# Kernel tuning notes

Measured on AMD Instinct MI355X. Metric: run time of the kernel, lower is better.

Reference implementation:

```python
import jax, jax.numpy as jnp
import numpy as np

B, S, OBS, D, H, F, L, A = 64, 512, 128, 512, 8, 2048, 4, 16
KERNEL_EPS = 1e-3  # performer kernel_epsilon
LN_EPS = 1e-6      # flax LayerNorm default


def _layernorm(x, s, b):
    m = jnp.mean(x, axis=-1, keepdims=True)
    v = jnp.mean(jnp.square(x - m), axis=-1, keepdims=True)
    return (x - m) * jax.lax.rsqrt(v + LN_EPS) * s + b


def _favor_attn(x, Wq, bq, Wk, bk, Wv, bv, Wo, bo):
    # FAVOR+ generalized attention, deterministic relu features, bidirectional,
    # renormalize_attention=True. phi(u) = relu(u) + kernel_epsilon.
    Bx, Sx, Dx = x.shape
    hd = Dx // H
    q = (x @ Wq + bq).reshape(Bx, Sx, H, hd)
    k = (x @ Wk + bk).reshape(Bx, Sx, H, hd)
    v = (x @ Wv + bv).reshape(Bx, Sx, H, hd)
    pq = jax.nn.relu(q) + KERNEL_EPS  # [B,S,H,m]
    pk = jax.nn.relu(k) + KERNEL_EPS
    kv = jnp.einsum('bshm,bshd->bhmd', pk, v)      # [B,H,m,hd]
    num = jnp.einsum('bshm,bhmd->bshd', pq, kv)    # [B,S,H,hd]
    ksum = jnp.sum(pk, axis=1)                      # [B,H,m]
    den = jnp.einsum('bshm,bhm->bsh', pq, ksum)    # [B,S,H]
    out = num / den[..., None]
    return out.reshape(Bx, Sx, Dx) @ Wo + bo


def setup_inputs() -> dict:
    key = jax.random.key(0)
    ks = jax.random.split(key, 32)
    sc = lambda *shape: 0.02
    inp = {
        'hidden_state': jax.random.normal(ks[0], (B, 1, D), jnp.float32),
        'ins': jax.random.normal(ks[1], (B, S, OBS), jnp.float32),
        'resets': jax.random.randint(ks[2], (B,), 0, 2) > 0,
        'W_emb': jax.random.normal(ks[3], (OBS, D), jnp.float32) * 0.02,
        'b_emb': jnp.zeros((D,), jnp.float32),
        'Wq': jax.random.normal(ks[4], (L, D, D), jnp.float32) * 0.02,
        'bq': jnp.zeros((L, D), jnp.float32),
        'Wk': jax.random.normal(ks[5], (L, D, D), jnp.float32) * 0.02,
        'bk': jnp.zeros((L, D), jnp.float32),
        'Wv': jax.random.normal(ks[6], (L, D, D), jnp.float32) * 0.02,
        'bv': jnp.zeros((L, D), jnp.float32),
        'Wo': jax.random.normal(ks[7], (L, D, D), jnp.float32) * 0.02,
        'bo': jnp.zeros((L, D), jnp.float32),
        'ln1_s': jnp.ones((L, D), jnp.float32),
        'ln1_b': jnp.zeros((L, D), jnp.float32),
        'ln2_s': jnp.ones((L, D), jnp.float32),
        'ln2_b': jnp.zeros((L, D), jnp.float32),
        'W1': jax.random.normal(ks[8], (L, D, F), jnp.float32) * 0.02,
        'b1': jnp.zeros((L, F), jnp.float32),
        'W2': jax.random.normal(ks[9], (L, F, D), jnp.float32) * 0.02,
        'b2': jnp.zeros((L, D), jnp.float32),
        'W_qp': jax.random.normal(ks[10], (D, A), jnp.float32) * 0.02,
        'b_qp': jnp.zeros((A,), jnp.float32),
    }
    return inp


def reference(hidden_state, ins, resets, W_emb, b_emb, Wq, bq, Wk, bk, Wv, bv,
              Wo, bo, ln1_s, ln1_b, ln2_s, ln2_b, W1, b1, W2, b2, W_qp, b_qp):
    emb = ins @ W_emb + b_emb                                   # [B,S,D]
    h0 = jnp.where(resets[:, None, None], jnp.zeros_like(hidden_state), hidden_state)
    x = jnp.concatenate([h0, emb], axis=1)                      # [B,S+1,D]
    for l in range(Wq.shape[0]):
        att = _favor_attn(x, Wq[l], bq[l], Wk[l], bk[l], Wv[l], bv[l], Wo[l], bo[l])
        x = _layernorm(att + x, ln1_s[l], ln1_b[l])
        ff = jax.nn.relu(x @ W1[l] + b1[l]) @ W2[l] + b2[l]
        x = _layernorm(ff + x, ln2_s[l], ln2_b[l])
    h_out = x[:, 0:1, :]                                        # [B,1,D]
    q_vals = h_out @ W_qp + b_qp                                # [B,1,A]
    return (h_out, q_vals)
```

## Files before the change

### kernel.cpp

```cpp
#include <hip/hip_runtime.h>

typedef __bf16 bf16;
typedef __bf16 bf16x8 __attribute__((ext_vector_type(8)));
typedef float  f32x4  __attribute__((ext_vector_type(4)));


__device__ __forceinline__ void cp16(const bf16* g, bf16* l)
{
    __builtin_amdgcn_global_load_lds(
        (const __attribute__((address_space(1))) void*)g,
        (__attribute__((address_space(3))) void*)l,
        16, 0, 0);
}

__global__ __launch_bounds__(256) void cvt_bf16(
    const float* __restrict__ src, bf16* __restrict__ dst, int n)
{
    for (int i = blockIdx.x * 256 + threadIdx.x; i < n; i += gridDim.x * 256)
        dst[i] = (bf16)src[i];
}

__global__ __launch_bounds__(256) void transpose_f32(
    const float* __restrict__ W, bf16* __restrict__ WT, int K, int N, long elemOff)
{
    __shared__ bf16 tile[32][33];
    const int bn = blockIdx.x * 32;
    const int bk = blockIdx.y * 32;
    const int tx = threadIdx.x & 31, ty = threadIdx.x >> 5;
    for (int r = 0; r < 32; r += 8)
        tile[ty + r][tx] = (bf16)W[elemOff + (long)(bk + ty + r) * N + (bn + tx)];
    __syncthreads();
    for (int r = 0; r < 32; r += 8)
        WT[(long)(bn + ty + r) * K + (bk + tx)] = tile[tx][ty + r];
}

__global__ __launch_bounds__(256) void build_x0(
    const float* __restrict__ hs, const int* __restrict__ resets,
    bf16* __restrict__ xb)
{
    const int b = blockIdx.x;
    const bool rz = (resets[b] != 0);
    const long base = (long)b * 513 * 512;
    for (int d = threadIdx.x; d < 512; d += 256)
        xb[base + d] = rz ? (bf16)0.f : (bf16)hs[b * 512 + d];
}

__global__ __launch_bounds__(256) void concat3(
    const float* __restrict__ a, const float* __restrict__ b,
    const float* __restrict__ c, float* __restrict__ d)
{
    const int i = blockIdx.x * 256 + threadIdx.x;
    if (i < 512)       d[i] = a[i];
    else if (i < 1024) d[i] = b[i - 512];
    else if (i < 1536) d[i] = c[i - 1024];
}

template<int ROWMAP, int ACT>
__global__ __launch_bounds__(256) void gemm128(
    const bf16* __restrict__ A, const bf16* __restrict__ BT,
    const float* __restrict__ bias, bf16* __restrict__ outB,
    int M, int N, int K, int lda, int ldc)
{
    __shared__ bf16 As[128 * 32];
    __shared__ bf16 Bs[128 * 32];
    const int tid  = threadIdx.x;
    const int wave = tid >> 6;
    const int lane = tid & 63;
    const int q    = lane >> 4;
    const int lm   = lane & 15;
    const int wr   = wave >> 1, wc = wave & 1;

    int flat;
    {
        const int nwg  = gridDim.x * gridDim.y;
        const int orig = blockIdx.y * gridDim.x + blockIdx.x;
        const int qq = nwg >> 3, rr = nwg & 7;
        const int xcd = orig & 7, idx = orig >> 3;
        flat = (xcd < rr ? xcd * (qq + 1) : rr * (qq + 1) + (xcd - rr) * qq) + idx;
    }
    const int bx = flat % gridDim.x;
    const int by = flat / gridDim.x;
    int m0 = by * 128;
    if (m0 > M - 128) m0 = M - 128;
    const int n0 = bx * 128;

    const int r0 = wave * 32 + (lane >> 2);
    const int ks = (lane & 3) * 8;
    const bf16* Ag0 = A  + (long)(m0 + r0) * lda + ks;
    const bf16* Ag1 = A  + (long)(m0 + r0 + 16) * lda + ks;
    const bf16* Bg0 = BT + (long)(n0 + r0) * K + ks;
    const bf16* Bg1 = BT + (long)(n0 + r0 + 16) * K + ks;
    bf16* Al0 = As + wave * 1024;
    bf16* Al1 = As + wave * 1024 + 512;
    bf16* Bl0 = Bs + wave * 1024;
    bf16* Bl1 = Bs + wave * 1024 + 512;

    f32x4 acc[4][4];
    for (int i = 0; i < 4; i++) for (int j = 0; j < 4; j++)
        for (int r = 0; r < 4; r++) acc[i][j][r] = 0.f;

    for (int k0 = 0; k0 < K; k0 += 32) {
        cp16(Ag0 + k0, Al0);
        cp16(Ag1 + k0, Al1);
        cp16(Bg0 + k0, Bl0);
        cp16(Bg1 + k0, Bl1);
        __syncthreads();
        bf16x8 af[4], bfr[4];
        #pragma unroll
        for (int i = 0; i < 4; i++)
            af[i] = *(const bf16x8*)(As + (wr * 64 + i * 16 + lm) * 32 + q * 8);
        #pragma unroll
        for (int j = 0; j < 4; j++)
            bfr[j] = *(const bf16x8*)(Bs + (wc * 64 + j * 16 + lm) * 32 + q * 8);
        #pragma unroll
        for (int i = 0; i < 4; i++)
            #pragma unroll
            for (int j = 0; j < 4; j++)
                acc[i][j] = __builtin_amdgcn_mfma_f32_16x16x32_bf16(
                    af[i], bfr[j], acc[i][j], 0, 0, 0);
        __syncthreads();
    }

    #pragma unroll
    for (int j = 0; j < 4; j++) {
        const int col = n0 + wc * 64 + j * 16 + lm;
        const float bv = bias[col];
        #pragma unroll
        for (int i = 0; i < 4; i++) {
            #pragma unroll
            for (int r = 0; r < 4; r++) {
                int row = m0 + wr * 64 + i * 16 + q * 4 + r;
                float vv = acc[i][j][r] + bv;
                if (ACT == 1) vv = fmaxf(vv, 0.f);
                if (ACT == 2) vv = fmaxf(vv, 0.f) + 1e-3f;
                if (ACT == 3 && col < 1024) vv = fmaxf(vv, 0.f) + 1e-3f;
                if (ROWMAP == 1) row = row + (row >> 9) + 1;
                outB[(long)row * ldc + col] = (bf16)vv;
            }
        }
    }
}

#define FP 72
__global__ __launch_bounds__(256) void favor_mfma(bf16* qkv)
{
    const int bh = blockIdx.x;
    const int b = bh >> 3, h = bh & 7;
    const long rbQ = (long)b * 513 * 1536 + h * 64;
    const long rbK = rbQ + 512;
    const long rbV = rbQ + 1024;

    __shared__ bf16 pkT[64][FP];
    __shared__ bf16 vT [64][FP];
    __shared__ bf16 kvT[64][FP];
    __shared__ bf16 pqS[64][FP];
    __shared__ float ksumS[64];
    __shared__ float denS[64];

    const int tid  = threadIdx.x;
    const int wave = tid >> 6;
    const int lane = tid & 63;
    const int q    = lane >> 4;
    const int lm   = lane & 15;
    const int wr   = wave >> 1, wc = wave & 1;
    const int mp   = (tid & 31) * 2;
    const int sr   = tid >> 5;

    if (tid < 64) ksumS[tid] = 0.f;
    float ksp0 = 0.f, ksp1 = 0.f;

    f32x4 akv[2][2];
    for (int i = 0; i < 2; i++) for (int j = 0; j < 2; j++)
        for (int r = 0; r < 4; r++) akv[i][j][r] = 0.f;

    for (int t8 = 0; t8 < 9; t8++) {
        const int s0 = t8 * 64;
        #pragma unroll
        for (int i = 0; i < 8; i++) {
            const int s  = sr + i * 8;
            const int gs = s0 + s;
            unsigned pkw = 0, vw = 0;
            if (gs < 513) {
                pkw = *(const unsigned*)(qkv + rbK + (long)gs * 1536 + mp);
                vw  = *(const unsigned*)(qkv + rbV + (long)gs * 1536 + mp);
            }
            union { unsigned u; bf16 hh[2]; } pu, vu;
            pu.u = pkw; vu.u = vw;
            pkT[mp][s]     = pu.hh[0];
            pkT[mp + 1][s] = pu.hh[1];
            vT[mp][s]      = vu.hh[0];
            vT[mp + 1][s]  = vu.hh[1];
            ksp0 += (float)pu.hh[0];
            ksp1 += (float)pu.hh[1];
        }
        __syncthreads();
        #pragma unroll
        for (int ks = 0; ks < 2; ks++) {
            bf16x8 a0 = *(const bf16x8*)(&pkT[wr * 32 + lm     ][ks * 32 + q * 8]);
            bf16x8 a1 = *(const bf16x8*)(&pkT[wr * 32 + 16 + lm][ks * 32 + q * 8]);
            bf16x8 b0 = *(const bf16x8*)(&vT [wc * 32 + lm     ][ks * 32 + q * 8]);
            bf16x8 b1 = *(const bf16x8*)(&vT [wc * 32 + 16 + lm][ks * 32 + q * 8]);
            akv[0][0] = __builtin_amdgcn_mfma_f32_16x16x32_bf16(a0, b0, akv[0][0], 0, 0, 0);
            akv[0][1] = __builtin_amdgcn_mfma_f32_16x16x32_bf16(a0, b1, akv[0][1], 0, 0, 0);
            akv[1][0] = __builtin_amdgcn_mfma_f32_16x16x32_bf16(a1, b0, akv[1][0], 0, 0, 0);
            akv[1][1] = __builtin_amdgcn_mfma_f32_16x16x32_bf16(a1, b1, akv[1][1], 0, 0, 0);
        }
        __syncthreads();
    }
    atomicAdd(&ksumS[mp],     ksp0);
    atomicAdd(&ksumS[mp + 1], ksp1);
    #pragma unroll
    for (int i = 0; i < 2; i++)
        #pragma unroll
        for (int j = 0; j < 2; j++)
            #pragma unroll
            for (int r = 0; r < 4; r++)
                kvT[wc * 32 + j * 16 + lm][wr * 32 + i * 16 + q * 4 + r] =
                    (bf16)akv[i][j][r];
    __syncthreads();

    const int prow = tid >> 2;
    const int pseg = (tid & 3) * 16;
    for (int t8 = 0; t8 < 9; t8++) {
        const int s0 = t8 * 64;
        const int gs = s0 + prow;
        if (gs < 513) {
            *(bf16x8*)(&pqS[prow][pseg])     = *(const bf16x8*)(qkv + rbQ + (long)gs * 1536 + pseg);
            *(bf16x8*)(&pqS[prow][pseg + 8]) = *(const bf16x8*)(qkv + rbQ + (long)gs * 1536 + pseg + 8);
        } else {
            bf16x8 z;
            for (int r = 0; r < 8; r++) z[r] = (bf16)0.f;
            *(bf16x8*)(&pqS[prow][pseg])     = z;
            *(bf16x8*)(&pqS[prow][pseg + 8]) = z;
        }
        __syncthreads();
        {
            const int s = tid >> 2, mb = (tid & 3) * 16;
            float dp = 0.f;
            #pragma unroll
            for (int m2 = 0; m2 < 16; m2++)
                dp += (float)pqS[s][mb + m2] * ksumS[mb + m2];
            dp += __shfl_xor(dp, 1);
            dp += __shfl_xor(dp, 2);
            if ((tid & 3) == 0) denS[s] = dp;
        }
        __syncthreads();
        f32x4 an[4];
        for (int j = 0; j < 4; j++)
            for (int r = 0; r < 4; r++) an[j][r] = 0.f;
        #pragma unroll
        for (int ks = 0; ks < 2; ks++) {
            bf16x8 a = *(const bf16x8*)(&pqS[wave * 16 + lm][ks * 32 + q * 8]);
            #pragma unroll
            for (int j = 0; j < 4; j++) {
                bf16x8 bb = *(const bf16x8*)(&kvT[j * 16 + lm][ks * 32 + q * 8]);
                an[j] = __builtin_amdgcn_mfma_f32_16x16x32_bf16(a, bb, an[j], 0, 0, 0);
            }
        }
        #pragma unroll
        for (int j = 0; j < 4; j++) {
            #pragma unroll
            for (int r = 0; r < 4; r++) {
                const int sl  = wave * 16 + q * 4 + r;
                const int gs2 = s0 + sl;
                if (gs2 < 513) {
                    const int d = j * 16 + lm;
                    qkv[rbQ + (long)gs2 * 1536 + d] = (bf16)(an[j][r] / denS[sl]);
                }
            }
        }
        __syncthreads();
    }
}

__global__ __launch_bounds__(256) void ln_res(
    const bf16* __restrict__ y, int ldy, const float* __restrict__ sc,
    const float* __restrict__ bi, bf16* __restrict__ xb)
{
    const int row  = blockIdx.x * 4 + (threadIdx.x >> 6);
    const int lane = threadIdx.x & 63;
    const bf16* yr = y  + (long)row * ldy + lane * 8;
    bf16*       xr = xb + (long)row * 512 + lane * 8;
    bf16x8 yv = *(const bf16x8*)yr;
    bf16x8 xv = *(const bf16x8*)xr;
    float v[8];
    float sum = 0.f;
    #pragma unroll
    for (int i = 0; i < 8; i++) { v[i] = (float)yv[i] + (float)xv[i]; sum += v[i]; }
    #pragma unroll
    for (int o = 32; o; o >>= 1) sum += __shfl_xor(sum, o);
    const float mean = sum * (1.f / 512.f);
    float vs = 0.f;
    #pragma unroll
    for (int i = 0; i < 8; i++) { float dd = v[i] - mean; vs += dd * dd; }
    #pragma unroll
    for (int o = 32; o; o >>= 1) vs += __shfl_xor(vs, o);
    const float rstd = rsqrtf(vs * (1.f / 512.f) + 1e-6f);
    bf16x8 ov;
    #pragma unroll
    for (int i = 0; i < 8; i++)
        ov[i] = (bf16)((v[i] - mean) * rstd * sc[lane * 8 + i] + bi[lane * 8 + i]);
    *(bf16x8*)xr = ov;
}

__global__ __launch_bounds__(256) void final_head(
    const bf16* __restrict__ xb, const float* __restrict__ Wqp,
    const float* __restrict__ bqp, float* __restrict__ out)
{
    const int b = blockIdx.x;
    const bf16* xr = xb + (long)b * 513 * 512;
    for (int i = threadIdx.x; i < 512; i += 256) out[b * 512 + i] = (float)xr[i];
    const int a = threadIdx.x & 15, g = threadIdx.x >> 4;
    float p = 0.f;
    for (int k = g * 32; k < g * 32 + 32; k++)
        p += (float)xr[k] * Wqp[k * 16 + a];
    __shared__ float red[256];
    red[threadIdx.x] = p;
    __syncthreads();
    if (threadIdx.x < 16) {
        float s = bqp[a];
        for (int g2 = 0; g2 < 16; g2++) s += red[g2 * 16 + a];
        out[64 * 512 + b * 16 + a] = s;
    }
}

extern "C" void kernel_launch(void* const* d_in, const int* in_sizes, int n_in,
                              void* d_out, int out_size, void* d_ws, size_t ws_size,
                              hipStream_t stream)
{
    (void)in_sizes; (void)n_in; (void)out_size; (void)ws_size;
    const float* hs    = (const float*)d_in[0];
    const float* ins   = (const float*)d_in[1];
    const int*   resets= (const int*)d_in[2];
    const float* W_emb = (const float*)d_in[3];
    const float* b_emb = (const float*)d_in[4];
    const float* Wq    = (const float*)d_in[5];
    const float* bq    = (const float*)d_in[6];
    const float* Wk    = (const float*)d_in[7];
    const float* bk    = (const float*)d_in[8];
    const float* Wv    = (const float*)d_in[9];
    const float* bv    = (const float*)d_in[10];
    const float* Wo    = (const float*)d_in[11];
    const float* bo    = (const float*)d_in[12];
    const float* ln1s  = (const float*)d_in[13];
    const float* ln1b  = (const float*)d_in[14];
    const float* ln2s  = (const float*)d_in[15];
    const float* ln2b  = (const float*)d_in[16];
    const float* W1    = (const float*)d_in[17];
    const float* b1    = (const float*)d_in[18];
    const float* W2    = (const float*)d_in[19];
    const float* b2    = (const float*)d_in[20];
    const float* Wqp   = (const float*)d_in[21];
    const float* bqp   = (const float*)d_in[22];
    float* out = (float*)d_out;
    char* ws  = (char*)d_ws;

    bf16* xb   = (bf16*)(ws);
    bf16* qkv  = (bf16*)(ws + 33619968);
    bf16* f    = qkv;
    bf16* y2   = (bf16*)(ws + 33619968 + 67239936);
    bf16* WembT= (bf16*)(ws + 134479872);
    char* LW   = ws + 134610944;
    bf16* WqkvT= (bf16*)(LW + 0);
    bf16* WoT  = (bf16*)(LW + 1572864);
    bf16* W1T  = (bf16*)(LW + 2097152);
    bf16* W2T  = (bf16*)(LW + 4194304);
    float* bqkv= (float*)(LW + 6291456);
    bf16* insb = (bf16*)(ws + 140908544);

    cvt_bf16<<<4096, 256, 0, stream>>>(ins, insb, 4194304);
    transpose_f32<<<dim3(16, 4), 256, 0, stream>>>(W_emb, WembT, 128, 512, 0);
    build_x0<<<64, 256, 0, stream>>>(hs, resets, xb);
    gemm128<1, 0><<<dim3(4, 256), 256, 0, stream>>>(
        insb, WembT, b_emb, xb, 32768, 512, 128, 128, 512);

    for (int l = 0; l < 4; l++) {
        const long o512  = (long)l * 262144;
        const long o2048 = (long)l * 1048576;
        transpose_f32<<<dim3(16, 16), 256, 0, stream>>>(Wq, WqkvT,          512, 512,  o512);
        transpose_f32<<<dim3(16, 16), 256, 0, stream>>>(Wk, WqkvT + 262144, 512, 512,  o512);
        transpose_f32<<<dim3(16, 16), 256, 0, stream>>>(Wv, WqkvT + 524288, 512, 512,  o512);
        transpose_f32<<<dim3(16, 16), 256, 0, stream>>>(Wo, WoT,            512, 512,  o512);
        transpose_f32<<<dim3(64, 16), 256, 0, stream>>>(W1, W1T,            512, 2048, o2048);
        transpose_f32<<<dim3(16, 64), 256, 0, stream>>>(W2, W2T,            2048, 512, o2048);
        concat3<<<6, 256, 0, stream>>>(bq + l * 512, bk + l * 512, bv + l * 512, bqkv);

        gemm128<0, 3><<<dim3(12, 257), 256, 0, stream>>>(
            xb, WqkvT, bqkv, qkv, 32832, 1536, 512, 512, 1536);
        favor_mfma<<<512, 256, 0, stream>>>(qkv);
        gemm128<0, 0><<<dim3(4, 257), 256, 0, stream>>>(
            qkv, WoT, bo + l * 512, qkv + 512, 32832, 512, 512, 1536, 1536);
        ln_res<<<8208, 256, 0, stream>>>(qkv + 512, 1536, ln1s + l * 512, ln1b + l * 512, xb);

        for (int c = 0; c < 2; c++) {
            const long r0 = (long)c * 16416;
            gemm128<0, 1><<<dim3(16, 129), 256, 0, stream>>>(
                xb + r0 * 512, W1T, b1 + l * 2048, f, 16416, 2048, 512, 512, 2048);
            gemm128<0, 0><<<dim3(4, 129), 256, 0, stream>>>(
                f, W2T, b2 + l * 512, y2 + r0 * 512, 16416, 512, 2048, 2048, 512);
        }
        ln_res<<<8208, 256, 0, stream>>>(y2, 512, ln2s + l * 512, ln2b + l * 512, xb);
    }

    final_head<<<64, 256, 0, stream>>>(xb, Wqp, bqp, out);
}
```

Measured before the change: 1.906 ms.

## Widen GEMM K-tile to 64 and batch per-layer weight prep launches

The bf16 MFMA GEMM now stages 64-wide K tiles per iteration: eight async global-to-LDS copies per wave and two MFMA sub-steps between barriers. This halves the number of loop iterations and barriers and keeps more loads in flight. The per-layer weight transposes are merged into two z-indexed launches, and the QKV bias concat is hoisted into a single launch over all layers, reusing the WembT scratch area once the embedding GEMM is done. The GEMM doubles its LDS use, and the 128-byte LDS row stride may add bank conflicts on fragment reads.

```diff
diff --git a/kernel.cpp b/kernel.cpp
--- a/kernel.cpp
+++ b/kernel.cpp
@@ -32,6 +32,63 @@
     __syncthreads();
     for (int r = 0; r < 32; r += 8)
         WT[(long)(bn + ty + r) * K + (bk + tx)] = tile[tx][ty + r];
+}
+
+__global__ __launch_bounds__(256) void prep_qkvo(
+    const float* __restrict__ Wq, const float* __restrict__ Wk,
+    const float* __restrict__ Wv, const float* __restrict__ Wo,
+    bf16* __restrict__ WqkvT, bf16* __restrict__ WoT, long elemOff)
+{
+    __shared__ bf16 tile[32][33];
+    const int z = blockIdx.z;
+    const float* W = (z == 0) ? Wq : (z == 1) ? Wk : (z == 2) ? Wv : Wo;
+    bf16* WT = (z < 3) ? (WqkvT + (long)z * 262144) : WoT;
+    const int bn = blockIdx.x * 32;
+    const int bk = blockIdx.y * 32;
+    const int tx = threadIdx.x & 31, ty = threadIdx.x >> 5;
+    for (int r = 0; r < 32; r += 8)
+        tile[ty + r][tx] = (bf16)W[elemOff + (long)(bk + ty + r) * 512 + (bn + tx)];
+    __syncthreads();
+    for (int r = 0; r < 32; r += 8)
+        WT[(long)(bn + ty + r) * 512 + (bk + tx)] = tile[tx][ty + r];
+}
+
+__global__ __launch_bounds__(256) void prep_ffn(
+    const float* __restrict__ W1, const float* __restrict__ W2,
+    bf16* __restrict__ W1T, bf16* __restrict__ W2T, long elemOff)
+{
+    __shared__ bf16 tile[32][33];
+    const int z = blockIdx.z;
+    const float* W = z ? W2 : W1;
+    bf16* WT = z ? W2T : W1T;
+    const int N = z ? 512 : 2048;
+    const int K = z ? 2048 : 512;
+    const int bn = (z ? blockIdx.y : blockIdx.x) * 32;
+    const int bk = (z ? blockIdx.x : blockIdx.y) * 32;
+    const int tx = threadIdx.x & 31, ty = threadIdx.x >> 5;
+    for (int r = 0; r < 32; r += 8)
+        tile[ty + r][tx] = (bf16)W[elemOff + (long)(bk + ty + r) * N + (bn + tx)];
+    __syncthreads();
+    for (int r = 0; r < 32; r += 8)
+        WT[(long)(bn + ty + r) * K + (bk + tx)] = tile[tx][ty + r];
+}
+
+__global__ __launch_bounds__(256) void concat_all(
+    const float* __restrict__ bq, const float* __restrict__ bk,
+    const float* __restrict__ bv, float* __restrict__ dst)
+{
+    const int i = blockIdx.x * 256 + threadIdx.x;
+    const int l = i >> 11;
+    int rem = i;
+    int lay = 0;
+    while (rem >= 1536) { rem -= 1536; lay++; }
+    if (lay > 3) return;
+    float v;
+    if (rem < 512)        v = bq[lay * 512 + rem];
+    else if (rem < 1024)  v = bk[lay * 512 + rem - 512];
+    else                  v = bv[lay * 512 + rem - 1024];
+    dst[lay * 1536 + rem] = v;
+    (void)l;
 }
 
 __global__ __launch_bounds__(256) void build_x0(
@@ -45,24 +102,14 @@
         xb[base + d] = rz ? (bf16)0.f : (bf16)hs[b * 512 + d];
 }
 
-__global__ __launch_bounds__(256) void concat3(
-    const float* __restrict__ a, const float* __restrict__ b,
-    const float* __restrict__ c, float* __restrict__ d)
-{
-    const int i = blockIdx.x * 256 + threadIdx.x;
-    if (i < 512)       d[i] = a[i];
-    else if (i < 1024) d[i] = b[i - 512];
-    else if (i < 1536) d[i] = c[i - 1024];
-}
-
 template<int ROWMAP, int ACT>
 __global__ __launch_bounds__(256) void gemm128(
     const bf16* __restrict__ A, const bf16* __restrict__ BT,
     const float* __restrict__ bias, bf16* __restrict__ outB,
     int M, int N, int K, int lda, int ldc)
 {
-    __shared__ bf16 As[128 * 32];
-    __shared__ bf16 Bs[128 * 32];
+    __shared__ bf16 As[128 * 64];
+    __shared__ bf16 Bs[128 * 64];
     const int tid  = threadIdx.x;
     const int wave = tid >> 6;
     const int lane = tid & 63;
@@ -84,40 +131,42 @@
     if (m0 > M - 128) m0 = M - 128;
     const int n0 = bx * 128;
 
-    const int r0 = wave * 32 + (lane >> 2);
-    const int ks = (lane & 3) * 8;
-    const bf16* Ag0 = A  + (long)(m0 + r0) * lda + ks;
-    const bf16* Ag1 = A  + (long)(m0 + r0 + 16) * lda + ks;
-    const bf16* Bg0 = BT + (long)(n0 + r0) * K + ks;
-    const bf16* Bg1 = BT + (long)(n0 + r0 + 16) * K + ks;
-    bf16* Al0 = As + wave * 1024;
-    bf16* Al1 = As + wave * 1024 + 512;
-    bf16* Bl0 = Bs + wave * 1024;
-    bf16* Bl1 = Bs + wave * 1024 + 512;
+    const int srow = lane >> 3;
+    const int scol = (lane & 7) * 8;
+    const bf16* Ag = A  + (long)(m0 + wave * 32 + srow) * lda + scol;
+    const bf16* Bg = BT + (long)(n0 + wave * 32 + srow) * K   + scol;
+    const long lda8 = (long)lda * 8;
+    const long K8   = (long)K * 8;
+    bf16* Al = As + wave * 2048;
+    bf16* Bl = Bs + wave * 2048;
 
     f32x4 acc[4][4];
     for (int i = 0; i < 4; i++) for (int j = 0; j < 4; j++)
         for (int r = 0; r < 4; r++) acc[i][j][r] = 0.f;
 
-    for (int k0 = 0; k0 < K; k0 += 32) {
-        cp16(Ag0 + k0, Al0);
-        cp16(Ag1 + k0, Al1);
-        cp16(Bg0 + k0, Bl0);
-        cp16(Bg1 + k0, Bl1);
-        __syncthreads();
-        bf16x8 af[4], bfr[4];
-        #pragma unroll
-        for (int i = 0; i < 4; i++)
-            af[i] = *(const bf16x8*)(As + (wr * 64 + i * 16 + lm) * 32 + q * 8);
-        #pragma unroll
-        for (int j = 0; j < 4; j++)
-            bfr[j] = *(const bf16x8*)(Bs + (wc * 64 + j * 16 + lm) * 32 + q * 8);
-        #pragma unroll
-        for (int i = 0; i < 4; i++)
+    for (int k0 = 0; k0 < K; k0 += 64) {
+        #pragma unroll
+        for (int i = 0; i < 4; i++) {
+            cp16(Ag + i * lda8 + k0, Al + i * 512);
+            cp16(Bg + i * K8   + k0, Bl + i * 512);
+        }
+        __syncthreads();
+        #pragma unroll
+        for (int ks = 0; ks < 2; ks++) {
+            bf16x8 af[4], bfr[4];
+            #pragma unroll
+            for (int i = 0; i < 4; i++)
+                af[i] = *(const bf16x8*)(As + (wr * 64 + i * 16 + lm) * 64 + ks * 32 + q * 8);
             #pragma unroll
             for (int j = 0; j < 4; j++)
-                acc[i][j] = __builtin_amdgcn_mfma_f32_16x16x32_bf16(
-                    af[i], bfr[j], acc[i][j], 0, 0, 0);
+                bfr[j] = *(const bf16x8*)(Bs + (wc * 64 + j * 16 + lm) * 64 + ks * 32 + q * 8);
+            #pragma unroll
+            for (int i = 0; i < 4; i++)
+                #pragma unroll
+                for (int j = 0; j < 4; j++)
+                    acc[i][j] = __builtin_amdgcn_mfma_f32_16x16x32_bf16(
+                        af[i], bfr[j], acc[i][j], 0, 0, 0);
+        }
         __syncthreads();
     }
 
@@ -360,12 +409,12 @@
     bf16* f    = qkv;
     bf16* y2   = (bf16*)(ws + 33619968 + 67239936);
     bf16* WembT= (bf16*)(ws + 134479872);
+    float* bqkv_all = (float*)(ws + 134479872);
     char* LW   = ws + 134610944;
     bf16* WqkvT= (bf16*)(LW + 0);
     bf16* WoT  = (bf16*)(LW + 1572864);
     bf16* W1T  = (bf16*)(LW + 2097152);
     bf16* W2T  = (bf16*)(LW + 4194304);
-    float* bqkv= (float*)(LW + 6291456);
     bf16* insb = (bf16*)(ws + 140908544);
 
     cvt_bf16<<<4096, 256, 0, stream>>>(ins, insb, 4194304);
@@ -373,20 +422,16 @@
     build_x0<<<64, 256, 0, stream>>>(hs, resets, xb);
     gemm128<1, 0><<<dim3(4, 256), 256, 0, stream>>>(
         insb, WembT, b_emb, xb, 32768, 512, 128, 128, 512);
+    concat_all<<<24, 256, 0, stream>>>(bq, bk, bv, bqkv_all);
 
     for (int l = 0; l < 4; l++) {
         const long o512  = (long)l * 262144;
         const long o2048 = (long)l * 1048576;
-        transpose_f32<<<dim3(16, 16), 256, 0, stream>>>(Wq, WqkvT,          512, 512,  o512);
-        transpose_f32<<<dim3(16, 16), 256, 0, stream>>>(Wk, WqkvT + 262144, 512, 512,  o512);
-        transpose_f32<<<dim3(16, 16), 256, 0, stream>>>(Wv, WqkvT + 524288, 512, 512,  o512);
-        transpose_f32<<<dim3(16, 16), 256, 0, stream>>>(Wo, WoT,            512, 512,  o512);
-        transpose_f32<<<dim3(64, 16), 256, 0, stream>>>(W1, W1T,            512, 2048, o2048);
-        transpose_f32<<<dim3(16, 64), 256, 0, stream>>>(W2, W2T,            2048, 512, o2048);
-        concat3<<<6, 256, 0, stream>>>(bq + l * 512, bk + l * 512, bv + l * 512, bqkv);
+        prep_qkvo<<<dim3(16, 16, 4), 256, 0, stream>>>(Wq, Wk, Wv, Wo, WqkvT, WoT, o512);
+        prep_ffn<<<dim3(64, 16, 2), 256, 0, stream>>>(W1, W2, W1T, W2T, o2048);
 
         gemm128<0, 3><<<dim3(12, 257), 256, 0, stream>>>(
-            xb, WqkvT, bqkv, qkv, 32832, 1536, 512, 512, 1536);
+            xb, WqkvT, bqkv_all + l * 1536, qkv, 32832, 1536, 512, 512, 1536);
         favor_mfma<<<512, 256, 0, stream>>>(qkv);
         gemm128<0, 0><<<dim3(4, 257), 256, 0, stream>>>(
             qkv, WoT, bo + l * 512, qkv + 512, 32832, 512, 512, 1536, 1536);
```

New measurement: 2.263 ms. +18.7%, slower.
